# Kernel tuning notes

Measured on AMD Instinct MI355X. Metric: run time of the kernel, lower is better.

Reference implementation:

```python
import jax, jax.numpy as jnp
import numpy as np

N_NODES = 100000
N_EDGES = 1600000
B = 256
H = 512
HEADS = 8
DH = H // HEADS


def setup_inputs() -> dict:
    key = jax.random.key(0)
    ks = list(jax.random.split(key, 24))
    def nrm(i, shape, s=0.02):
        return jax.random.normal(ks[i], shape, jnp.float32) * s
    inp = {}
    inp["text_features"] = jax.random.normal(ks[0], (B, 768), jnp.float32)
    inp["video_features"] = jax.random.normal(ks[1], (B, 512), jnp.float32)
    inp["x"] = jax.random.normal(ks[2], (N_NODES, 64), jnp.float32)
    inp["edge_index"] = jax.random.randint(ks[3], (2, N_EDGES), 0, N_NODES, dtype=jnp.int32)
    # sorted node->graph assignment covering all B graphs (no empty segments)
    inp["batch_idx"] = ((jnp.arange(N_NODES) * B) // N_NODES).astype(jnp.int32)
    inp["Wt"] = nrm(4, (768, H)); inp["bt"] = jnp.zeros((H,), jnp.float32)
    inp["Wv"] = nrm(5, (512, H)); inp["bv"] = jnp.zeros((H,), jnp.float32)
    inp["Wq"] = nrm(6, (H, H)); inp["bq"] = jnp.zeros((H,), jnp.float32)
    inp["Wk"] = nrm(7, (H, H)); inp["bk"] = jnp.zeros((H,), jnp.float32)
    inp["Wva"] = nrm(8, (H, H)); inp["bva"] = jnp.zeros((H,), jnp.float32)
    inp["Wo"] = nrm(9, (H, H)); inp["bo"] = jnp.zeros((H,), jnp.float32)
    inp["Wf"] = nrm(10, (2 * H, H)); inp["bf"] = jnp.zeros((H,), jnp.float32)
    inp["G1W"] = nrm(11, (64, 128)); inp["G1b"] = jnp.zeros((128,), jnp.float32)
    inp["G2W"] = nrm(12, (128, 128)); inp["G2b"] = jnp.zeros((128,), jnp.float32)
    inp["G3W"] = nrm(13, (128, 256)); inp["G3b"] = jnp.zeros((256,), jnp.float32)
    inp["Wff"] = nrm(14, (H + 256, H)); inp["bff"] = jnp.zeros((H,), jnp.float32)
    inp["Wb"] = nrm(15, (H, 2)); inp["bb"] = jnp.zeros((2,), jnp.float32)
    inp["Wa"] = nrm(16, (H, 2)); inp["ba"] = jnp.zeros((2,), jnp.float32)
    return inp


def _gcn_conv(h, W, b, src, dst, dis):
    # PyG GCNConv: linear transform, symmetric-normalized aggregation w/ self-loops, bias
    hw = h @ W                                       # [N, C]
    norm = dis[src] * dis[dst]                       # [E]
    msg = hw[src] * norm[:, None]                    # [E, C]
    agg = jax.ops.segment_sum(msg, dst, num_segments=h.shape[0])
    agg = agg + hw * (dis * dis)[:, None]            # self-loop messages
    return agg + b


def reference(text_features, video_features, x, edge_index, batch_idx, Wt, bt, Wv, bv, Wq, bq, Wk, bk, Wva, bva, Wo, bo, Wf, bf, G1W, G1b, G2W, G2b, G3W, G3b, Wff, bff, Wb, bb, Wa, ba):
    # encoders (dropout is eval-mode no-op)
    text_enc = jax.nn.relu(text_features @ Wt + bt)      # [B, H]
    video_enc = jax.nn.relu(video_features @ Wv + bv)    # [B, H]
    # multihead attention; torch seq lens are both 1 (batch acts as N)
    q = (text_enc @ Wq + bq).reshape(B, HEADS, 1, DH)
    k = (video_enc @ Wk + bk).reshape(B, HEADS, 1, DH)
    v = (video_enc @ Wva + bva).reshape(B, HEADS, 1, DH)
    scores = jnp.einsum('bhqd,bhkd->bhqk', q, k) / np.float32(np.sqrt(DH))
    w = jax.nn.softmax(scores, axis=-1)
    attn = jnp.einsum('bhqk,bhkd->bhqd', w, v).reshape(B, H)
    text_attended = attn @ Wo + bo
    # multimodal fusion
    fused = jax.nn.relu(jnp.concatenate([text_attended, video_enc], axis=1) @ Wf + bf)
    # GCN stack
    src, dst = edge_index[0], edge_index[1]
    deg = jax.ops.segment_sum(jnp.ones((N_EDGES,), jnp.float32), dst, num_segments=N_NODES) + 1.0
    dis = jax.lax.rsqrt(deg)
    h = jax.nn.elu(_gcn_conv(x, G1W, G1b, src, dst, dis))
    h = jax.nn.elu(_gcn_conv(h, G2W, G2b, src, dst, dis))
    h = _gcn_conv(h, G3W, G3b, src, dst, dis)            # [N, 256]
    # per-graph mean pooling (the original per-batch Python loop, as one segment-mean)
    counts = jax.ops.segment_sum(jnp.ones((N_NODES,), jnp.float32), batch_idx, num_segments=B)
    pooled = jax.ops.segment_sum(h, batch_idx, num_segments=B) / counts[:, None]  # [B, 256]
    # final fusion + classifier heads
    final = jax.nn.relu(jnp.concatenate([fused, pooled], axis=1) @ Wff + bff)
    bullying = jax.nn.log_softmax(final @ Wb + bb, axis=1)
    aggression = jax.nn.log_softmax(final @ Wa + ba, axis=1)
    return bullying, aggression
```

## Files before the change

kernel.cpp:

```cpp
#include <hip/hip_runtime.h>
#include <hip/hip_bf16.h>

#define N_NODES 100000
#define NPAD    100096
#define N_EDGES 1600000
#define BATCH   256
#define HDIM    512

typedef unsigned short u16;
typedef __attribute__((ext_vector_type(8))) short bf16x8;
typedef __attribute__((ext_vector_type(8))) unsigned short u16x8;
typedef __attribute__((ext_vector_type(4))) float f32x4;

__device__ __forceinline__ float bf2f(u16 u) {
    union { unsigned i; float f; } v; v.i = ((unsigned)u) << 16; return v.f;
}
__device__ __forceinline__ u16 f2bf(float f) {
    __hip_bfloat16 h = __float2bfloat16(f);
    return *reinterpret_cast<u16*>(&h);
}

template<int K, int ACT, int SCALE>
__global__ __launch_bounds__(256) void gemm_mfma(
        const u16* __restrict__ A, const u16* __restrict__ Wt,
        const float* __restrict__ bias, const float* __restrict__ dis,
        u16* __restrict__ C, int N) {
    constexpr int RB = K * 2;
    __shared__ u16 As[128 * K];
    __shared__ u16 Bs[128 * K];
    const int tid  = threadIdx.x;
    const int lane = tid & 63;
    const int w    = tid >> 6;
    const int wr   = w >> 1, wc = w & 1;
    const int row0 = blockIdx.y * 128;
    const int col0 = blockIdx.x * 128;

    constexpr int WB     = 128 * RB / 4;
    constexpr int PASSES = WB / 1024;
    const size_t Abase = (size_t)row0 * K;
    const size_t Bbase = (size_t)col0 * K;
    #pragma unroll
    for (int p = 0; p < PASSES; ++p) {
        int Lb  = w * WB + p * 1024;
        int L   = Lb + lane * 16;
        int row = L / RB;
        int cb  = L % RB;
        int scb = cb ^ ((row & 7) << 4);
        const u16* ga = A  + Abase + (size_t)row * K + (scb >> 1);
        const u16* gb = Wt + Bbase + (size_t)row * K + (scb >> 1);
        __builtin_amdgcn_global_load_lds((const __attribute__((address_space(1))) void*)ga,
            (__attribute__((address_space(3))) void*)&As[Lb >> 1], 16, 0, 0);
        __builtin_amdgcn_global_load_lds((const __attribute__((address_space(1))) void*)gb,
            (__attribute__((address_space(3))) void*)&Bs[Lb >> 1], 16, 0, 0);
    }
    asm volatile("s_waitcnt vmcnt(0)" ::: "memory");
    __syncthreads();

    const int rl = lane & 15;
    const int kg = lane >> 4;
    f32x4 acc[4][4] = {};
    #pragma unroll
    for (int s = 0; s < K / 32; ++s) {
        bf16x8 af[4], bg[4];
        #pragma unroll
        for (int m = 0; m < 4; ++m) {
            int row = wr * 64 + m * 16 + rl;
            int cb  = s * 64 + kg * 16;
            int scb = cb ^ ((row & 7) << 4);
            af[m] = *(const bf16x8*)&As[(row * RB + scb) >> 1];
        }
        #pragma unroll
        for (int n = 0; n < 4; ++n) {
            int row = wc * 64 + n * 16 + rl;
            int cb  = s * 64 + kg * 16;
            int scb = cb ^ ((row & 7) << 4);
            bg[n] = *(const bf16x8*)&Bs[(row * RB + scb) >> 1];
        }
        #pragma unroll
        for (int m = 0; m < 4; ++m)
            #pragma unroll
            for (int n = 0; n < 4; ++n)
                acc[m][n] = __builtin_amdgcn_mfma_f32_16x16x32_bf16(af[m], bg[n], acc[m][n], 0, 0, 0);
    }

    #pragma unroll
    for (int m = 0; m < 4; ++m) {
        #pragma unroll
        for (int r = 0; r < 4; ++r) {
            int grow = row0 + wr * 64 + m * 16 + kg * 4 + r;
            float ds = SCALE ? dis[grow] : 1.f;
            #pragma unroll
            for (int n = 0; n < 4; ++n) {
                int gcol = col0 + wc * 64 + n * 16 + rl;
                float v = acc[m][n][r] + bias[gcol];
                if (ACT == 2) v = v > 0.f ? v : expm1f(v);
                C[(size_t)grow * N + gcol] = f2bf(v * ds);
            }
        }
    }
}

template<int ACT>
__global__ __launch_bounds__(256) void gemm_loop(
        const u16* __restrict__ A, const u16* __restrict__ Wt,
        const float* __restrict__ bias, u16* __restrict__ C,
        int N, int K, int lda, int ldc) {
    __shared__ u16 As[128 * 64];
    __shared__ u16 Bs[128 * 64];
    const int tid  = threadIdx.x;
    const int lane = tid & 63;
    const int w    = tid >> 6;
    const int wr   = w >> 1, wc = w & 1;
    const int row0 = blockIdx.y * 128;
    const int col0 = blockIdx.x * 128;
    const int rl = lane & 15;
    const int kg = lane >> 4;
    f32x4 acc[4][4] = {};

    for (int k0 = 0; k0 < K; k0 += 64) {
        #pragma unroll
        for (int p = 0; p < 4; ++p) {
            int Lb  = w * 4096 + p * 1024;
            int L   = Lb + lane * 16;
            int row = L >> 7;
            int cb  = L & 127;
            int scb = cb ^ ((row & 7) << 4);
            const u16* ga = A  + (size_t)(row0 + row) * lda + k0 + (scb >> 1);
            const u16* gb = Wt + (size_t)(col0 + row) * K   + k0 + (scb >> 1);
            __builtin_amdgcn_global_load_lds((const __attribute__((address_space(1))) void*)ga,
                (__attribute__((address_space(3))) void*)&As[Lb >> 1], 16, 0, 0);
            __builtin_amdgcn_global_load_lds((const __attribute__((address_space(1))) void*)gb,
                (__attribute__((address_space(3))) void*)&Bs[Lb >> 1], 16, 0, 0);
        }
        asm volatile("s_waitcnt vmcnt(0)" ::: "memory");
        __syncthreads();
        #pragma unroll
        for (int s = 0; s < 2; ++s) {
            bf16x8 af[4], bg[4];
            #pragma unroll
            for (int m = 0; m < 4; ++m) {
                int row = wr * 64 + m * 16 + rl;
                int cb  = s * 64 + kg * 16;
                int scb = cb ^ ((row & 7) << 4);
                af[m] = *(const bf16x8*)&As[(row * 128 + scb) >> 1];
            }
            #pragma unroll
            for (int n = 0; n < 4; ++n) {
                int row = wc * 64 + n * 16 + rl;
                int cb  = s * 64 + kg * 16;
                int scb = cb ^ ((row & 7) << 4);
                bg[n] = *(const bf16x8*)&Bs[(row * 128 + scb) >> 1];
            }
            #pragma unroll
            for (int m = 0; m < 4; ++m)
                #pragma unroll
                for (int n = 0; n < 4; ++n)
                    acc[m][n] = __builtin_amdgcn_mfma_f32_16x16x32_bf16(af[m], bg[n], acc[m][n], 0, 0, 0);
        }
        __syncthreads();
    }

    #pragma unroll
    for (int m = 0; m < 4; ++m) {
        #pragma unroll
        for (int r = 0; r < 4; ++r) {
            int grow = row0 + wr * 64 + m * 16 + kg * 4 + r;
            #pragma unroll
            for (int n = 0; n < 4; ++n) {
                int gcol = col0 + wc * 64 + n * 16 + rl;
                float v = acc[m][n][r] + bias[gcol];
                if (ACT == 1) v = fmaxf(v, 0.f);
                C[(size_t)grow * ldc + gcol] = f2bf(v);
            }
        }
    }
}

template<int K, int N>
__device__ __forceinline__ void tw(const float* __restrict__ W, u16* __restrict__ Wt, int t) {
    int n = t / K, k = t - n * K;
    Wt[t] = f2bf(W[(size_t)k * N + n]);
}

__global__ void prep(const float* __restrict__ G1W, u16* __restrict__ g1wt,
                     const float* __restrict__ G2W, u16* __restrict__ g2wt,
                     const float* __restrict__ Wv,  u16* __restrict__ WvT,
                     const float* __restrict__ Wva, u16* __restrict__ WvaT,
                     const float* __restrict__ Wo,  u16* __restrict__ WoT,
                     const float* __restrict__ Wf,  u16* __restrict__ WfT,
                     const float* __restrict__ video, u16* __restrict__ vidbf) {
    const int bid = blockIdx.x, tid = threadIdx.x;
    if (bid < 32)        { tw<64, 128>  (G1W, g1wt, bid * 256 + tid); }
    else if (bid < 96)   { tw<128, 128> (G2W, g2wt, (bid - 32) * 256 + tid); }
    else if (bid < 1120) { tw<512, 512> (Wv,  WvT,  (bid - 96) * 256 + tid); }
    else if (bid < 2144) { tw<512, 512> (Wva, WvaT, (bid - 1120) * 256 + tid); }
    else if (bid < 3168) { tw<512, 512> (Wo,  WoT,  (bid - 2144) * 256 + tid); }
    else if (bid < 5216) { tw<1024, 512>(Wf,  WfT,  (bid - 3168) * 256 + tid); }
    else { int t = (bid - 5216) * 256 + tid; vidbf[t] = f2bf(video[t]); }
}

__global__ void final_fused(const u16* __restrict__ fusedb,
                            const float* __restrict__ pooled, const float* __restrict__ counts,
                            const float* __restrict__ G3W, const float* __restrict__ G3b,
                            const float* __restrict__ Wff, const float* __restrict__ bff,
                            const float* __restrict__ Wb,  const float* __restrict__ bb,
                            const float* __restrict__ Wa,  const float* __restrict__ ba,
                            float* __restrict__ out) {
    __shared__ float cat[768], fin[512], pp[128];
    __shared__ float rd[4][4];
    const int b = blockIdx.x, tid = threadIdx.x;
    cat[tid] = bf2f(fusedb[b * 512 + tid]);
    cat[tid + 256] = bf2f(fusedb[b * 512 + 256 + tid]);
    float inv = 1.f / counts[b];
    if (tid < 128) pp[tid] = pooled[b * 128 + tid] * inv;
    __syncthreads();
    {
        float s = G3b[tid];
        #pragma unroll 8
        for (int k = 0; k < 128; ++k) s += pp[k] * G3W[k * 256 + tid];
        cat[512 + tid] = s;
    }
    __syncthreads();
    {
        float a0 = bff[tid], a1 = bff[tid + 256];
        #pragma unroll 8
        for (int k = 0; k < 768; ++k) {
            float xv = cat[k];
            a0 += xv * Wff[k * 512 + tid];
            a1 += xv * Wff[k * 512 + tid + 256];
        }
        fin[tid] = fmaxf(a0, 0.f);
        fin[tid + 256] = fmaxf(a1, 0.f);
    }
    __syncthreads();
    float z0 = 0.f, z1 = 0.f, y0 = 0.f, y1 = 0.f;
    for (int k = tid; k < 512; k += 256) {
        float f = fin[k];
        z0 += f * Wb[2 * k];
        z1 += f * Wb[2 * k + 1];
        y0 += f * Wa[2 * k];
        y1 += f * Wa[2 * k + 1];
    }
    #pragma unroll
    for (int off = 32; off > 0; off >>= 1) {
        z0 += __shfl_down(z0, off);
        z1 += __shfl_down(z1, off);
        y0 += __shfl_down(y0, off);
        y1 += __shfl_down(y1, off);
    }
    int ww = tid >> 6;
    if ((tid & 63) == 0) { rd[ww][0] = z0; rd[ww][1] = z1; rd[ww][2] = y0; rd[ww][3] = y1; }
    __syncthreads();
    if (tid == 0) {
        float Z0 = rd[0][0] + rd[1][0] + rd[2][0] + rd[3][0] + bb[0];
        float Z1 = rd[0][1] + rd[1][1] + rd[2][1] + rd[3][1] + bb[1];
        float Y0 = rd[0][2] + rd[1][2] + rd[2][2] + rd[3][2] + ba[0];
        float Y1 = rd[0][3] + rd[1][3] + rd[2][3] + rd[3][3] + ba[1];
        float m = fmaxf(Z0, Z1);
        float l = m + logf(expf(Z0 - m) + expf(Z1 - m));
        out[b * 2 + 0] = Z0 - l;
        out[b * 2 + 1] = Z1 - l;
        float m2 = fmaxf(Y0, Y1);
        float l2 = m2 + logf(expf(Y0 - m2) + expf(Y1 - m2));
        out[512 + b * 2 + 0] = Y0 - l2;
        out[512 + b * 2 + 1] = Y1 - l2;
    }
}

__global__ void deg_slot(const int* __restrict__ dstE, int* __restrict__ deg,
                         int* __restrict__ slot, int E) {
    int e = blockIdx.x * blockDim.x + threadIdx.x;
    if (e < E) slot[e] = atomicAdd(&deg[dstE[e]], 1);
}

__global__ void scan1(const int* __restrict__ in, int* __restrict__ out,
                      int* __restrict__ bsum, float* __restrict__ dis, int n) {
    __shared__ int ts[256];
    const int tid = threadIdx.x;
    const int base = blockIdx.x * 1024;
    int v[4];
    #pragma unroll
    for (int i = 0; i < 4; ++i) {
        int idx = base + tid * 4 + i;
        v[i] = (idx < n) ? in[idx] : 0;
        if (idx < NPAD) dis[idx] = rsqrtf((float)v[i] + 1.f);
    }
    ts[tid] = v[0] + v[1] + v[2] + v[3];
    __syncthreads();
    for (int off = 1; off < 256; off <<= 1) {
        int val = (tid >= off) ? ts[tid - off] : 0;
        __syncthreads();
        ts[tid] += val;
        __syncthreads();
    }
    int run = (tid == 0) ? 0 : ts[tid - 1];
    if (tid == 255) bsum[blockIdx.x] = ts[255];
    #pragma unroll
    for (int i = 0; i < 4; ++i) {
        int idx = base + tid * 4 + i;
        if (idx < n) out[idx] = run;
        run += v[i];
    }
}

__global__ void scan2(int* __restrict__ bsum, int nb) {
    int l = threadIdx.x;
    int a = (l < nb) ? bsum[l] : 0;
    int b = (l + 64 < nb) ? bsum[l + 64] : 0;
    int oa = a, ob = b;
    #pragma unroll
    for (int off = 1; off < 64; off <<= 1) {
        int t = __shfl_up(a, off);
        if (l >= off) a += t;
    }
    int totA = __shfl(a, 63);
    #pragma unroll
    for (int off = 1; off < 64; off <<= 1) {
        int t = __shfl_up(b, off);
        if (l >= off) b += t;
    }
    if (l < nb) bsum[l] = a - oa;
    if (l + 64 < nb) bsum[l + 64] = totA + b - ob;
}

__global__ void scan3(int* __restrict__ out, const int* __restrict__ bsum, int n, int total) {
    int idx = blockIdx.x * 1024 + threadIdx.x * 4;
    int add = bsum[blockIdx.x];
    #pragma unroll
    for (int i = 0; i < 4; ++i)
        if (idx + i < n) out[idx + i] += add;
    if (blockIdx.x == 0 && threadIdx.x == 0) out[n] = total;
}

__global__ void csr_scatter2(const int* __restrict__ srcE, const int* __restrict__ dstE,
                             const int* __restrict__ rowptr, const int* __restrict__ slot,
                             int* __restrict__ csr_src, int E) {
    int e = blockIdx.x * blockDim.x + threadIdx.x;
    if (e >= E) return;
    csr_src[rowptr[dstE[e]] + slot[e]] = srcE[e];
}

__global__ void scale_rows64_bf16(const float* __restrict__ x, const float* __restrict__ dis,
                                  u16* __restrict__ out) {
    int t = blockIdx.x * blockDim.x + threadIdx.x;
    if (t >= N_NODES * 64) return;
    out[t] = f2bf(x[t] * dis[t >> 6]);
}

template<int C>
__global__ void csr_agg_bf16(const u16* __restrict__ Hs, const int* __restrict__ rowptr,
                             const int* __restrict__ csr_src, const float* __restrict__ dis,
                             u16* __restrict__ out) {
    constexpr int LPG = C / 8;
    constexpr int G   = 64 / LPG;
    int node = blockIdx.x * 4 + (threadIdx.x >> 6);
    if (node >= N_NODES) return;
    int lane = threadIdx.x & 63;
    int g  = lane / LPG;
    int cl = lane % LPG;
    int s0 = rowptr[node], s1 = rowptr[node + 1];
    float a[8] = {};
    if (g == 0) {
        u16x8 v = *(const u16x8*)&Hs[(size_t)node * C + cl * 8];
        #pragma unroll
        for (int j = 0; j < 8; ++j) a[j] = bf2f(v[j]);
    }
    int e = s0 + g;
    while (e + G < s1) {
        int sA = csr_src[e], sB = csr_src[e + G];
        u16x8 vA = *(const u16x8*)&Hs[(size_t)sA * C + cl * 8];
        u16x8 vB = *(const u16x8*)&Hs[(size_t)sB * C + cl * 8];
        #pragma unroll
        for (int j = 0; j < 8; ++j) a[j] += bf2f(vA[j]) + bf2f(vB[j]);
        e += 2 * G;
    }
    while (e < s1) {
        int s = csr_src[e];
        u16x8 v = *(const u16x8*)&Hs[(size_t)s * C + cl * 8];
        #pragma unroll
        for (int j = 0; j < 8; ++j) a[j] += bf2f(v[j]);
        e += G;
    }
    #pragma unroll
    for (int m = LPG; m < 64; m <<= 1)
        #pragma unroll
        for (int j = 0; j < 8; ++j) a[j] += __shfl_xor(a[j], m);
    if (g == 0) {
        float dd = dis[node];
        u16x8 o;
        #pragma unroll
        for (int j = 0; j < 8; ++j) o[j] = f2bf(a[j] * dd);
        *(u16x8*)&out[(size_t)node * C + cl * 8] = o;
    }
}

__global__ __launch_bounds__(256) void csr_agg_pool(
        const u16* __restrict__ Hs, const int* __restrict__ rowptr,
        const int* __restrict__ csr_src, const float* __restrict__ dis,
        const int* __restrict__ batch,
        float* __restrict__ pooled, float* __restrict__ counts) {
    __shared__ float bins[2][128];
    __shared__ int cnt[2];
    const int tid = threadIdx.x;
    const int base = blockIdx.x * 16;
    if (tid < 128) { bins[0][tid] = 0.f; bins[1][tid] = 0.f; }
    if (tid < 2) cnt[tid] = 0;
    __syncthreads();
    const int lane = tid & 63;
    const int w = tid >> 6;
    const int g = lane >> 4;
    const int cl = lane & 15;
    const int b0 = batch[base];
    #pragma unroll
    for (int i = 0; i < 4; ++i) {
        const int node = base + w * 4 + i;
        const int s0 = rowptr[node], s1 = rowptr[node + 1];
        float a[8] = {};
        if (g == 0) {
            u16x8 v = *(const u16x8*)&Hs[(size_t)node * 128 + cl * 8];
            #pragma unroll
            for (int j = 0; j < 8; ++j) a[j] = bf2f(v[j]);
        }
        int e = s0 + g;
        while (e + 4 < s1) {
            int sA = csr_src[e], sB = csr_src[e + 4];
            u16x8 vA = *(const u16x8*)&Hs[(size_t)sA * 128 + cl * 8];
            u16x8 vB = *(const u16x8*)&Hs[(size_t)sB * 128 + cl * 8];
            #pragma unroll
            for (int j = 0; j < 8; ++j) a[j] += bf2f(vA[j]) + bf2f(vB[j]);
            e += 8;
        }
        while (e < s1) {
            int s = csr_src[e];
            u16x8 v = *(const u16x8*)&Hs[(size_t)s * 128 + cl * 8];
            #pragma unroll
            for (int j = 0; j < 8; ++j) a[j] += bf2f(v[j]);
            e += 4;
        }
        #pragma unroll
        for (int m = 16; m < 64; m <<= 1)
            #pragma unroll
            for (int j = 0; j < 8; ++j) a[j] += __shfl_xor(a[j], m);
        if (g == 0) {
            int bin = (batch[node] != b0) ? 1 : 0;
            float dd = dis[node];
            #pragma unroll
            for (int j = 0; j < 8; ++j) atomicAdd(&bins[bin][cl * 8 + j], a[j] * dd);
            if (cl == 0) atomicAdd(&cnt[bin], 1);
        }
    }
    __syncthreads();
    int bin = tid >> 7, c = tid & 127;
    if (cnt[bin] > 0) atomicAdd(&pooled[(b0 + bin) * 128 + c], bins[bin][c]);
    if (tid < 2 && cnt[tid] > 0) atomicAdd(&counts[b0 + tid], (float)cnt[tid]);
}

extern "C" void kernel_launch(void* const* d_in, const int* in_sizes, int n_in,
                              void* d_out, int out_size, void* d_ws, size_t ws_size,
                              hipStream_t stream) {
    const float* video = (const float*)d_in[1];
    const float* x     = (const float*)d_in[2];
    const int*   eidx  = (const int*)d_in[3];
    const int*   batch = (const int*)d_in[4];
    const float* Wv  = (const float*)d_in[7],  *bv  = (const float*)d_in[8];
    const float* Wva = (const float*)d_in[13], *bva = (const float*)d_in[14];
    const float* Wo  = (const float*)d_in[15], *bo  = (const float*)d_in[16];
    const float* Wf  = (const float*)d_in[17], *bf  = (const float*)d_in[18];
    const float* G1W = (const float*)d_in[19], *G1b = (const float*)d_in[20];
    const float* G2W = (const float*)d_in[21], *G2b = (const float*)d_in[22];
    const float* G3W = (const float*)d_in[23], *G3b = (const float*)d_in[24];
    const float* Wff = (const float*)d_in[25], *bff = (const float*)d_in[26];
    const float* Wb  = (const float*)d_in[27], *bb  = (const float*)d_in[28];
    const float* Wa  = (const float*)d_in[29], *ba  = (const float*)d_in[30];
    const int* srcE = eidx;
    const int* dstE = eidx + N_EDGES;

    char* wsc = (char*)d_ws;
    size_t off = 0;
    auto alloc = [&](size_t bytes) { char* p = wsc + off; off += (bytes + 255) & ~(size_t)255; return p; };
    u16*   bufA   = (u16*)  alloc((size_t)NPAD * 128 * 2);
    u16*   bufB   = (u16*)  alloc((size_t)NPAD * 128 * 2);
    float* dis    = (float*)alloc(NPAD * 4);
    int*   deg    = (int*)  alloc(NPAD * 4);
    int*   rowptr = (int*)  alloc((N_NODES + 1) * 4);
    int*   slot   = (int*)  alloc((size_t)N_EDGES * 4);
    int*   csrsrc = (int*)  alloc((size_t)N_EDGES * 4);
    int*   bsum   = (int*)  alloc(128 * 4);
    u16*   g1wt   = (u16*)  alloc(128 * 64 * 2);
    u16*   g2wt   = (u16*)  alloc(128 * 128 * 2);
    u16*   WvT    = (u16*)  alloc(512 * 512 * 2);
    u16*   WvaT   = (u16*)  alloc(512 * 512 * 2);
    u16*   WoT    = (u16*)  alloc(512 * 512 * 2);
    u16*   WfT    = (u16*)  alloc(512 * 1024 * 2);
    u16*   vidbf  = (u16*)  alloc(BATCH * 512 * 2);
    u16*   catb   = (u16*)  alloc(BATCH * 1024 * 2);
    u16*   vattnb = (u16*)  alloc(BATCH * 512 * 2);
    u16*   fusedb = (u16*)  alloc(BATCH * 512 * 2);
    float* pooled = (float*)alloc((BATCH * 128 + BATCH) * 4);
    float* counts = pooled + BATCH * 128;

    const int NB = (N_NODES + 1023) / 1024;
    const int aggGrid = (N_NODES + 3) / 4;

    hipMemsetAsync(deg, 0, NPAD * 4, stream);
    hipMemsetAsync(pooled, 0, (BATCH * 128 + BATCH) * 4, stream);
    deg_slot<<<(N_EDGES + 255) / 256, 256, 0, stream>>>(dstE, deg, slot, N_EDGES);
    scan1<<<NB, 256, 0, stream>>>(deg, rowptr, bsum, dis, N_NODES);
    scan2<<<1, 64, 0, stream>>>(bsum, NB);
    scan3<<<NB, 256, 0, stream>>>(rowptr, bsum, N_NODES, N_EDGES);
    csr_scatter2<<<(N_EDGES + 255) / 256, 256, 0, stream>>>(srcE, dstE, rowptr, slot, csrsrc, N_EDGES);

    prep<<<5728, 256, 0, stream>>>(G1W, g1wt, G2W, g2wt, Wv, WvT, Wva, WvaT,
                                   Wo, WoT, Wf, WfT, video, vidbf);

    dim3 feGrid(4, 2);
    gemm_loop<1><<<feGrid, 256, 0, stream>>>(vidbf, WvT, bv, catb + 512, 512, 512, 512, 1024);
    gemm_loop<0><<<feGrid, 256, 0, stream>>>(catb + 512, WvaT, bva, vattnb, 512, 512, 1024, 512);
    gemm_loop<0><<<feGrid, 256, 0, stream>>>(vattnb, WoT, bo, catb, 512, 512, 512, 1024);
    gemm_loop<1><<<feGrid, 256, 0, stream>>>(catb, WfT, bf, fusedb, 512, 1024, 1024, 512);

    scale_rows64_bf16<<<(N_NODES * 64 + 255) / 256, 256, 0, stream>>>(x, dis, bufA);
    csr_agg_bf16<64><<<aggGrid, 256, 0, stream>>>(bufA, rowptr, csrsrc, dis, bufB);
    gemm_mfma<64, 2, 1><<<dim3(1, NPAD / 128), 256, 0, stream>>>(bufB, g1wt, G1b, dis, bufA, 128);
    csr_agg_bf16<128><<<aggGrid, 256, 0, stream>>>(bufA, rowptr, csrsrc, dis, bufB);
    gemm_mfma<128, 2, 1><<<dim3(1, NPAD / 128), 256, 0, stream>>>(bufB, g2wt, G2b, dis, bufA, 128);
    csr_agg_pool<<<N_NODES / 16, 256, 0, stream>>>(bufA, rowptr, csrsrc, dis, batch, pooled, counts);

    final_fused<<<BATCH, 256, 0, stream>>>(fusedb, pooled, counts, G3W, G3b,
                                           Wff, bff, Wb, bb, Wa, ba, (float*)d_out);
}
```

Measured before the change: 478.2 us.

## Merge degree counting into prep, fold scan3 into scatter, smaller dense GEMM tiles, deeper agg unroll

Merges the degree/slot atomic pass into the weight-prep kernel, and folds the rowptr offset add (scan3) into the CSR scatter kernel, removing two launches. The small 256x512 dense GEMMs switch from 128x128 tiles (8 blocks) to 64x64 tiles (32 blocks) to spread work over more CUs. The CSR aggregation loops are unrolled to four outstanding neighbor gathers instead of two to raise memory-level parallelism. The trade-offs are more register pressure in the aggregation loop and an extra global lookup of the block sum per edge in the scatter.

```diff
diff --git a/kernel.cpp b/kernel.cpp
--- a/kernel.cpp
+++ b/kernel.cpp
@@ -101,26 +101,26 @@
 }
 
 template<int ACT>
-__global__ __launch_bounds__(256) void gemm_loop(
+__global__ __launch_bounds__(256) void gemm64(
         const u16* __restrict__ A, const u16* __restrict__ Wt,
         const float* __restrict__ bias, u16* __restrict__ C,
-        int N, int K, int lda, int ldc) {
-    __shared__ u16 As[128 * 64];
-    __shared__ u16 Bs[128 * 64];
+        int K, int lda, int ldc) {
+    __shared__ u16 As[64 * 64];
+    __shared__ u16 Bs[64 * 64];
     const int tid  = threadIdx.x;
     const int lane = tid & 63;
     const int w    = tid >> 6;
     const int wr   = w >> 1, wc = w & 1;
-    const int row0 = blockIdx.y * 128;
-    const int col0 = blockIdx.x * 128;
+    const int row0 = blockIdx.y * 64;
+    const int col0 = blockIdx.x * 64;
     const int rl = lane & 15;
     const int kg = lane >> 4;
-    f32x4 acc[4][4] = {};
+    f32x4 acc[2][2] = {};
 
     for (int k0 = 0; k0 < K; k0 += 64) {
         #pragma unroll
-        for (int p = 0; p < 4; ++p) {
-            int Lb  = w * 4096 + p * 1024;
+        for (int p = 0; p < 2; ++p) {
+            int Lb  = w * 2048 + p * 1024;
             int L   = Lb + lane * 16;
             int row = L >> 7;
             int cb  = L & 127;
@@ -136,38 +136,38 @@
         __syncthreads();
         #pragma unroll
         for (int s = 0; s < 2; ++s) {
-            bf16x8 af[4], bg[4];
-            #pragma unroll
-            for (int m = 0; m < 4; ++m) {
-                int row = wr * 64 + m * 16 + rl;
+            bf16x8 af[2], bg[2];
+            #pragma unroll
+            for (int m = 0; m < 2; ++m) {
+                int row = wr * 32 + m * 16 + rl;
                 int cb  = s * 64 + kg * 16;
                 int scb = cb ^ ((row & 7) << 4);
                 af[m] = *(const bf16x8*)&As[(row * 128 + scb) >> 1];
             }
             #pragma unroll
-            for (int n = 0; n < 4; ++n) {
-                int row = wc * 64 + n * 16 + rl;
+            for (int n = 0; n < 2; ++n) {
+                int row = wc * 32 + n * 16 + rl;
                 int cb  = s * 64 + kg * 16;
                 int scb = cb ^ ((row & 7) << 4);
                 bg[n] = *(const bf16x8*)&Bs[(row * 128 + scb) >> 1];
             }
             #pragma unroll
-            for (int m = 0; m < 4; ++m)
+            for (int m = 0; m < 2; ++m)
                 #pragma unroll
-                for (int n = 0; n < 4; ++n)
+                for (int n = 0; n < 2; ++n)
                     acc[m][n] = __builtin_amdgcn_mfma_f32_16x16x32_bf16(af[m], bg[n], acc[m][n], 0, 0, 0);
         }
         __syncthreads();
     }
 
     #pragma unroll
-    for (int m = 0; m < 4; ++m) {
+    for (int m = 0; m < 2; ++m) {
         #pragma unroll
         for (int r = 0; r < 4; ++r) {
-            int grow = row0 + wr * 64 + m * 16 + kg * 4 + r;
-            #pragma unroll
-            for (int n = 0; n < 4; ++n) {
-                int gcol = col0 + wc * 64 + n * 16 + rl;
+            int grow = row0 + wr * 32 + m * 16 + kg * 4 + r;
+            #pragma unroll
+            for (int n = 0; n < 2; ++n) {
+                int gcol = col0 + wc * 32 + n * 16 + rl;
                 float v = acc[m][n][r] + bias[gcol];
                 if (ACT == 1) v = fmaxf(v, 0.f);
                 C[(size_t)grow * ldc + gcol] = f2bf(v);
@@ -182,14 +182,25 @@
     Wt[t] = f2bf(W[(size_t)k * N + n]);
 }
 
-__global__ void prep(const float* __restrict__ G1W, u16* __restrict__ g1wt,
-                     const float* __restrict__ G2W, u16* __restrict__ g2wt,
-                     const float* __restrict__ Wv,  u16* __restrict__ WvT,
-                     const float* __restrict__ Wva, u16* __restrict__ WvaT,
-                     const float* __restrict__ Wo,  u16* __restrict__ WoT,
-                     const float* __restrict__ Wf,  u16* __restrict__ WfT,
-                     const float* __restrict__ video, u16* __restrict__ vidbf) {
-    const int bid = blockIdx.x, tid = threadIdx.x;
+#define DEG_BLKS 6250
+
+__global__ void prep_deg(const int* __restrict__ dstE, int* __restrict__ deg,
+                         int* __restrict__ slot,
+                         const float* __restrict__ G1W, u16* __restrict__ g1wt,
+                         const float* __restrict__ G2W, u16* __restrict__ g2wt,
+                         const float* __restrict__ Wv,  u16* __restrict__ WvT,
+                         const float* __restrict__ Wva, u16* __restrict__ WvaT,
+                         const float* __restrict__ Wo,  u16* __restrict__ WoT,
+                         const float* __restrict__ Wf,  u16* __restrict__ WfT,
+                         const float* __restrict__ video, u16* __restrict__ vidbf) {
+    int bid = blockIdx.x;
+    const int tid = threadIdx.x;
+    if (bid < DEG_BLKS) {
+        int e = bid * 256 + tid;
+        slot[e] = atomicAdd(&deg[dstE[e]], 1);
+        return;
+    }
+    bid -= DEG_BLKS;
     if (bid < 32)        { tw<64, 128>  (G1W, g1wt, bid * 256 + tid); }
     else if (bid < 96)   { tw<128, 128> (G2W, g2wt, (bid - 32) * 256 + tid); }
     else if (bid < 1120) { tw<512, 512> (Wv,  WvT,  (bid - 96) * 256 + tid); }
@@ -267,12 +278,6 @@
     }
 }
 
-__global__ void deg_slot(const int* __restrict__ dstE, int* __restrict__ deg,
-                         int* __restrict__ slot, int E) {
-    int e = blockIdx.x * blockDim.x + threadIdx.x;
-    if (e < E) slot[e] = atomicAdd(&deg[dstE[e]], 1);
-}
-
 __global__ void scan1(const int* __restrict__ in, int* __restrict__ out,
                       int* __restrict__ bsum, float* __restrict__ dis, int n) {
     __shared__ int ts[256];
@@ -323,21 +328,16 @@
     if (l + 64 < nb) bsum[l + 64] = totA + b - ob;
 }
 
-__global__ void scan3(int* __restrict__ out, const int* __restrict__ bsum, int n, int total) {
-    int idx = blockIdx.x * 1024 + threadIdx.x * 4;
-    int add = bsum[blockIdx.x];
-    #pragma unroll
-    for (int i = 0; i < 4; ++i)
-        if (idx + i < n) out[idx + i] += add;
-    if (blockIdx.x == 0 && threadIdx.x == 0) out[n] = total;
-}
-
-__global__ void csr_scatter2(const int* __restrict__ srcE, const int* __restrict__ dstE,
-                             const int* __restrict__ rowptr, const int* __restrict__ slot,
-                             int* __restrict__ csr_src, int E) {
+__global__ void csr_scatter3(const int* __restrict__ srcE, const int* __restrict__ dstE,
+                             const int* __restrict__ partial, const int* __restrict__ bsum,
+                             const int* __restrict__ slot,
+                             int* __restrict__ csr_src, int* __restrict__ rowptr) {
     int e = blockIdx.x * blockDim.x + threadIdx.x;
-    if (e >= E) return;
-    csr_src[rowptr[dstE[e]] + slot[e]] = srcE[e];
+    if (e <= N_NODES) rowptr[e] = (e < N_NODES) ? (partial[e] + bsum[e >> 10]) : N_EDGES;
+    if (e < N_EDGES) {
+        int d = dstE[e];
+        csr_src[partial[d] + bsum[d >> 10] + slot[e]] = srcE[e];
+    }
 }
 
 __global__ void scale_rows64_bf16(const float* __restrict__ x, const float* __restrict__ dis,
@@ -366,13 +366,17 @@
         for (int j = 0; j < 8; ++j) a[j] = bf2f(v[j]);
     }
     int e = s0 + g;
-    while (e + G < s1) {
+    while (e + 3 * G < s1) {
         int sA = csr_src[e], sB = csr_src[e + G];
+        int sC = csr_src[e + 2 * G], sD = csr_src[e + 3 * G];
         u16x8 vA = *(const u16x8*)&Hs[(size_t)sA * C + cl * 8];
         u16x8 vB = *(const u16x8*)&Hs[(size_t)sB * C + cl * 8];
-        #pragma unroll
-        for (int j = 0; j < 8; ++j) a[j] += bf2f(vA[j]) + bf2f(vB[j]);
-        e += 2 * G;
+        u16x8 vC = *(const u16x8*)&Hs[(size_t)sC * C + cl * 8];
+        u16x8 vD = *(const u16x8*)&Hs[(size_t)sD * C + cl * 8];
+        #pragma unroll
+        for (int j = 0; j < 8; ++j)
+            a[j] += (bf2f(vA[j]) + bf2f(vB[j])) + (bf2f(vC[j]) + bf2f(vD[j]));
+        e += 4 * G;
     }
     while (e < s1) {
         int s = csr_src[e];
@@ -422,13 +426,17 @@
             for (int j = 0; j < 8; ++j) a[j] = bf2f(v[j]);
         }
         int e = s0 + g;
-        while (e + 4 < s1) {
+        while (e + 12 < s1) {
             int sA = csr_src[e], sB = csr_src[e + 4];
+            int sC = csr_src[e + 8], sD = csr_src[e + 12];
             u16x8 vA = *(const u16x8*)&Hs[(size_t)sA * 128 + cl * 8];
             u16x8 vB = *(const u16x8*)&Hs[(size_t)sB * 128 + cl * 8];
-            #pragma unroll
-            for (int j = 0; j < 8; ++j) a[j] += bf2f(vA[j]) + bf2f(vB[j]);
-            e += 8;
+            u16x8 vC = *(const u16x8*)&Hs[(size_t)sC * 128 + cl * 8];
+            u16x8 vD = *(const u16x8*)&Hs[(size_t)sD * 128 + cl * 8];
+            #pragma unroll
+            for (int j = 0; j < 8; ++j)
+                a[j] += (bf2f(vA[j]) + bf2f(vB[j])) + (bf2f(vC[j]) + bf2f(vD[j]));
+            e += 16;
         }
         while (e < s1) {
             int s = csr_src[e];
@@ -478,51 +486,50 @@
     char* wsc = (char*)d_ws;
     size_t off = 0;
     auto alloc = [&](size_t bytes) { char* p = wsc + off; off += (bytes + 255) & ~(size_t)255; return p; };
-    u16*   bufA   = (u16*)  alloc((size_t)NPAD * 128 * 2);
-    u16*   bufB   = (u16*)  alloc((size_t)NPAD * 128 * 2);
-    float* dis    = (float*)alloc(NPAD * 4);
-    int*   deg    = (int*)  alloc(NPAD * 4);
-    int*   rowptr = (int*)  alloc((N_NODES + 1) * 4);
-    int*   slot   = (int*)  alloc((size_t)N_EDGES * 4);
-    int*   csrsrc = (int*)  alloc((size_t)N_EDGES * 4);
-    int*   bsum   = (int*)  alloc(128 * 4);
-    u16*   g1wt   = (u16*)  alloc(128 * 64 * 2);
-    u16*   g2wt   = (u16*)  alloc(128 * 128 * 2);
-    u16*   WvT    = (u16*)  alloc(512 * 512 * 2);
-    u16*   WvaT   = (u16*)  alloc(512 * 512 * 2);
-    u16*   WoT    = (u16*)  alloc(512 * 512 * 2);
-    u16*   WfT    = (u16*)  alloc(512 * 1024 * 2);
-    u16*   vidbf  = (u16*)  alloc(BATCH * 512 * 2);
-    u16*   catb   = (u16*)  alloc(BATCH * 1024 * 2);
-    u16*   vattnb = (u16*)  alloc(BATCH * 512 * 2);
-    u16*   fusedb = (u16*)  alloc(BATCH * 512 * 2);
-    float* pooled = (float*)alloc((BATCH * 128 + BATCH) * 4);
-    float* counts = pooled + BATCH * 128;
+    u16*   bufA    = (u16*)  alloc((size_t)NPAD * 128 * 2);
+    u16*   bufB    = (u16*)  alloc((size_t)NPAD * 128 * 2);
+    float* dis     = (float*)alloc(NPAD * 4);
+    int*   deg     = (int*)  alloc(NPAD * 4);
+    int*   partial = (int*)  alloc(N_NODES * 4);
+    int*   rowptr  = (int*)  alloc((N_NODES + 1) * 4);
+    int*   slot    = (int*)  alloc((size_t)N_EDGES * 4);
+    int*   csrsrc  = (int*)  alloc((size_t)N_EDGES * 4);
+    int*   bsum    = (int*)  alloc(128 * 4);
+    u16*   g1wt    = (u16*)  alloc(128 * 64 * 2);
+    u16*   g2wt    = (u16*)  alloc(128 * 128 * 2);
+    u16*   WvT     = (u16*)  alloc(512 * 512 * 2);
+    u16*   WvaT    = (u16*)  alloc(512 * 512 * 2);
+    u16*   WoT     = (u16*)  alloc(512 * 512 * 2);
+    u16*   WfT     = (u16*)  alloc(512 * 1024 * 2);
+    u16*   vidbf   = (u16*)  alloc(BATCH * 512 * 2);
+    u16*   catb    = (u16*)  alloc(BATCH * 1024 * 2);
+    u16*   vattnb  = (u16*)  alloc(BATCH * 512 * 2);
+    u16*   fusedb  = (u16*)  alloc(BATCH * 512 * 2);
+    float* pooled  = (float*)alloc((BATCH * 128 + BATCH) * 4);
+    float* counts  = pooled + BATCH * 128;
 
     const int NB = (N_NODES + 1023) / 1024;
-    const int aggGrid = (N_NODES + 3) / 4;
 
     hipMemsetAsync(deg, 0, NPAD * 4, stream);
     hipMemsetAsync(pooled, 0, (BATCH * 128 + BATCH) * 4, stream);
-    deg_slot<<<(N_EDGES + 255) / 256, 256, 0, stream>>>(dstE, deg, slot, N_EDGES);
-    scan1<<<NB, 256, 0, stream>>>(deg, rowptr, bsum, dis, N_NODES);
+    prep_deg<<<DEG_BLKS + 5728, 256, 0, stream>>>(dstE, deg, slot,
+        G1W, g1wt, G2W, g2wt, Wv, WvT, Wva, WvaT, Wo, WoT, Wf, WfT, video, vidbf);
+
+    scan1<<<NB, 256, 0, stream>>>(deg, partial, bsum, dis, N_NODES);
     scan2<<<1, 64, 0, stream>>>(bsum, NB);
-    scan3<<<NB, 256, 0, stream>>>(rowptr, bsum, N_NODES, N_EDGES);
-    csr_scatter2<<<(N_EDGES + 255) / 256, 256, 0, stream>>>(srcE, dstE, rowptr, slot, csrsrc, N_EDGES);
-
-    prep<<<5728, 256, 0, stream>>>(G1W, g1wt, G2W, g2wt, Wv, WvT, Wva, WvaT,
-                                   Wo, WoT, Wf, WfT, video, vidbf);
-
-    dim3 feGrid(4, 2);
-    gemm_loop<1><<<feGrid, 256, 0, stream>>>(vidbf, WvT, bv, catb + 512, 512, 512, 512, 1024);
-    gemm_loop<0><<<feGrid, 256, 0, stream>>>(catb + 512, WvaT, bva, vattnb, 512, 512, 1024, 512);
-    gemm_loop<0><<<feGrid, 256, 0, stream>>>(vattnb, WoT, bo, catb, 512, 512, 512, 1024);
-    gemm_loop<1><<<feGrid, 256, 0, stream>>>(catb, WfT, bf, fusedb, 512, 1024, 1024, 512);
+    csr_scatter3<<<(N_EDGES + 255) / 256, 256, 0, stream>>>(srcE, dstE, partial, bsum,
+                                                            slot, csrsrc, rowptr);
+
+    dim3 fe512(8, 4);
+    gemm64<1><<<fe512, 256, 0, stream>>>(vidbf, WvT, bv, catb + 512, 512, 512, 1024);
+    gemm64<0><<<fe512, 256, 0, stream>>>(catb + 512, WvaT, bva, vattnb, 512, 1024, 512);
+    gemm64<0><<<fe512, 256, 0, stream>>>(vattnb, WoT, bo, catb, 512, 512, 1024);
+    gemm64<1><<<fe512, 256, 0, stream>>>(catb, WfT, bf, fusedb, 1024, 1024, 512);
 
     scale_rows64_bf16<<<(N_NODES * 64 + 255) / 256, 256, 0, stream>>>(x, dis, bufA);
-    csr_agg_bf16<64><<<aggGrid, 256, 0, stream>>>(bufA, rowptr, csrsrc, dis, bufB);
+    csr_agg_bf16<64><<<(N_NODES + 3) / 4, 256, 0, stream>>>(bufA, rowptr, csrsrc, dis, bufB);
     gemm_mfma<64, 2, 1><<<dim3(1, NPAD / 128), 256, 0, stream>>>(bufB, g1wt, G1b, dis, bufA, 128);
-    csr_agg_bf16<128><<<aggGrid, 256, 0, stream>>>(bufA, rowptr, csrsrc, dis, bufB);
+    csr_agg_bf16<128><<<(N_NODES + 3) / 4, 256, 0, stream>>>(bufA, rowptr, csrsrc, dis, bufB);
     gemm_mfma<128, 2, 1><<<dim3(1, NPAD / 128), 256, 0, stream>>>(bufB, g2wt, G2b, dis, bufA, 128);
     csr_agg_pool<<<N_NODES / 16, 256, 0, stream>>>(bufA, rowptr, csrsrc, dis, batch, pooled, counts);
 
```

Measured after the change: 448.0 us. -6.3%, faster.
